# Optimization experiments

Hardware: AMD Instinct MI355X
Metric: run time of the kernel (lower is better)

The kernel has to match this reference:

```python
import jax, jax.numpy as jnp
import numpy as np

NUM_HEADS = 12
HEAD_DIM = 64
MAX_POS = 1024  # max_position_embeddings


def setup_inputs() -> dict:
    key = jax.random.key(0)
    ks = jax.random.split(key, 6)
    B, S, H = 4, 1024, 768
    return {
        "hidden_states": jax.random.normal(ks[0], (B, S, H), dtype=jnp.float32),
        "attention_mask": jnp.zeros((B, 1, 1, S), dtype=jnp.float32),
        "Wq": jax.random.normal(ks[1], (H, H), dtype=jnp.float32) * 0.02,
        "bq": jnp.zeros((H,), dtype=jnp.float32),
        "Wk": jax.random.normal(ks[2], (H, H), dtype=jnp.float32) * 0.02,
        "bk": jnp.zeros((H,), dtype=jnp.float32),
        "Wv": jax.random.normal(ks[3], (H, H), dtype=jnp.float32) * 0.02,
        "bv": jnp.zeros((H,), dtype=jnp.float32),
        "dist_emb": jax.random.normal(ks[4], (2 * MAX_POS - 1, HEAD_DIM), dtype=jnp.float32) * 0.02,
    }


def _split_heads(x):
    # [B, S, H] -> [B, nh, S, hd]
    B, S, _ = x.shape
    return x.reshape(B, S, NUM_HEADS, HEAD_DIM).transpose(0, 2, 1, 3)


def reference(hidden_states, attention_mask, Wq, bq, Wk, bk, Wv, bv, dist_emb):
    B, S, H = hidden_states.shape
    q = _split_heads(hidden_states @ Wq + bq)  # [B, nh, S, hd]
    k = _split_heads(hidden_states @ Wk + bk)
    v = _split_heads(hidden_states @ Wv + bv)

    # raw scores QK^T: [B, nh, S, S]
    scores = jnp.einsum("bhld,bhrd->bhlr", q, k)

    # relative_key_query positional bias
    dist = jnp.arange(S)[:, None] - jnp.arange(S)[None, :] + MAX_POS - 1  # [S, S]
    pos = dist_emb[dist]  # [S, S, hd]
    scores = scores + jnp.einsum("bhld,lrd->bhlr", q, pos) \
                    + jnp.einsum("bhrd,lrd->bhlr", k, pos)

    scores = scores / jnp.sqrt(jnp.asarray(HEAD_DIM, scores.dtype))
    scores = scores + attention_mask  # additive mask broadcast [B,1,1,S]

    probs = jax.nn.softmax(scores, axis=-1)  # dropout prob = 0.0 (eval)
    ctx = jnp.einsum("bhlr,bhrd->bhld", probs, v)  # [B, nh, S, hd]
    ctx = ctx.transpose(0, 2, 1, 3).reshape(B, S, H)
    return ctx
```

## Files before the change

kernel.cpp:

```cpp
#include <hip/hip_runtime.h>

#define SEQ 1024
#define NH  12
#define HD  64
#define HID 768
#define NB  4

#define LOG2E  1.4426950408889634f
#define SC2    0.18033688011112042f
#define DTHR   11.541560327111707f

typedef short bf16x8 __attribute__((ext_vector_type(8)));
typedef float f32x16 __attribute__((ext_vector_type(16)));

#define LBAR() do {                                             \
    __builtin_amdgcn_sched_barrier(0);                          \
    asm volatile("s_waitcnt lgkmcnt(0)" ::: "memory");          \
    __builtin_amdgcn_s_barrier();                               \
    __builtin_amdgcn_sched_barrier(0);                          \
} while (0)

__device__ __forceinline__ unsigned short f2b(float f) {
    union { float f; unsigned u; } v; v.f = f;
    unsigned r = (v.u + 0x7FFFu + ((v.u >> 16) & 1u)) >> 16;
    return (unsigned short)r;
}
__device__ __forceinline__ float b2f(unsigned short s) {
    union { unsigned u; float f; } v; v.u = (unsigned)s << 16;
    return v.f;
}
__device__ __forceinline__ float g4(const float4& v, int e) {
    return e == 0 ? v.x : e == 1 ? v.y : e == 2 ? v.z : v.w;
}
__device__ __forceinline__ unsigned short u16g(const ushort4& v, int e) {
    return e == 0 ? v.x : e == 1 ? v.y : e == 2 ? v.z : v.w;
}

#define ROWFN(r, h) (((r) & 3) + 8 * ((r) >> 2) + 4 * (h))

#define NX4 786432
#define NE4 32752

__global__ void cvt_all(const float* __restrict__ X, const float* __restrict__ E,
                        unsigned short* __restrict__ Xb, unsigned short* __restrict__ Eb) {
    int i = blockIdx.x * blockDim.x + threadIdx.x;
    const int stride = gridDim.x * blockDim.x;
    for (; i < NX4 + NE4; i += stride) {
        float4 v;
        if (i < NX4) v = ((const float4*)X)[i];
        else         v = ((const float4*)E)[i - NX4];
        ushort4 o;
        o.x = f2b(v.x); o.y = f2b(v.y); o.z = f2b(v.z); o.w = f2b(v.w);
        if (i < NX4) ((ushort4*)Xb)[i] = o;
        else         ((ushort4*)Eb)[i - NX4] = o;
    }
}

__global__ __launch_bounds__(256) void cvt_wt(
    const float* __restrict__ Wq, const float* __restrict__ Wk, const float* __restrict__ Wv,
    unsigned short* __restrict__ Wt)
{
    __shared__ float T[64][65];
    const int z = blockIdx.z;
    const float* __restrict__ W = (z == 0) ? Wq : (z == 1) ? Wk : Wv;
    const int k0 = blockIdx.x * 64, n0 = blockIdx.y * 64;
    const int tid = threadIdx.x;
    #pragma unroll
    for (int ir = 0; ir < 4; ++ir) {
        int r = ir * 16 + (tid >> 4);
        int c4 = (tid & 15) * 4;
        *(float4*)&T[r][c4] = *(const float4*)&W[(size_t)(k0 + r) * HID + n0 + c4];
    }
    __syncthreads();
    const int cc = tid >> 2, q = tid & 3;
    unsigned short* dst = Wt + (size_t)z * HID * HID + (size_t)(n0 + cc) * HID + k0 + q * 16;
    #pragma unroll
    for (int j4 = 0; j4 < 4; ++j4) {
        ushort4 t4;
        t4.x = f2b(T[q * 16 + j4 * 4 + 0][cc]);
        t4.y = f2b(T[q * 16 + j4 * 4 + 1][cc]);
        t4.z = f2b(T[q * 16 + j4 * 4 + 2][cc]);
        t4.w = f2b(T[q * 16 + j4 * 4 + 3][cc]);
        *(ushort4*)(dst + j4 * 4) = t4;
    }
}

__global__ __launch_bounds__(256) void gemm_qkv(
    const unsigned short* __restrict__ Xb,
    const unsigned short* __restrict__ Wt,
    const float* __restrict__ bq, const float* __restrict__ bk, const float* __restrict__ bv,
    unsigned short* __restrict__ qkv)
{
    __shared__ unsigned short Xs[128][64];
    __shared__ unsigned short Ws[128][64];

    const int tid = threadIdx.x;
    const int lane = tid & 63;
    const int wid = tid >> 6;
    const int c = lane & 31;
    const int h2 = lane >> 5;
    const int m0 = blockIdx.x * 128, N0 = blockIdx.y * 128, z = blockIdx.z;
    const unsigned short* __restrict__ Wz = Wt + (size_t)z * HID * HID;
    const float* __restrict__ bias = (z == 0) ? bq : (z == 1) ? bk : bv;

    f32x16 acc[2][2];
    #pragma unroll
    for (int i = 0; i < 2; ++i)
        #pragma unroll
        for (int j = 0; j < 2; ++j)
            #pragma unroll
            for (int r = 0; r < 16; ++r) acc[i][j][r] = 0.f;

    for (int k0 = 0; k0 < HID; k0 += 64) {
        __syncthreads();
        #pragma unroll
        for (int it = 0; it < 4; ++it) {
            int t16 = tid + 256 * it;
            int row = t16 >> 3, s = t16 & 7;
            bf16x8 xv = *(const bf16x8*)(Xb + (size_t)(m0 + row) * HID + k0 + s * 8);
            *(bf16x8*)&Xs[row][(s ^ (row & 7)) * 8] = xv;
            bf16x8 wv = *(const bf16x8*)(Wz + (size_t)(N0 + row) * HID + k0 + s * 8);
            *(bf16x8*)&Ws[row][(s ^ (row & 7)) * 8] = wv;
        }
        __syncthreads();
        #pragma unroll
        for (int kc = 0; kc < 4; ++kc) {
            const int slot = kc * 2 + h2;
            bf16x8 af[2], bf_[2];
            #pragma unroll
            for (int i = 0; i < 2; ++i) {
                int ar = 64 * (wid >> 1) + 32 * i + c;
                int br = 64 * (wid & 1) + 32 * i + c;
                if (z != 2) {
                    af[i]  = *(const bf16x8*)&Xs[ar][(slot ^ (ar & 7)) * 8];
                    bf_[i] = *(const bf16x8*)&Ws[br][(slot ^ (br & 7)) * 8];
                } else {
                    af[i]  = *(const bf16x8*)&Ws[ar][(slot ^ (ar & 7)) * 8];
                    bf_[i] = *(const bf16x8*)&Xs[br][(slot ^ (br & 7)) * 8];
                }
            }
            #pragma unroll
            for (int i = 0; i < 2; ++i)
                #pragma unroll
                for (int j = 0; j < 2; ++j)
                    acc[i][j] = __builtin_amdgcn_mfma_f32_32x32x16_bf16(af[i], bf_[j], acc[i][j], 0, 0, 0);
        }
    }

    unsigned short* outz = qkv + (size_t)z * (NB * SEQ * HID);
    if (z != 2) {
        #pragma unroll
        for (int j = 0; j < 2; ++j) {
            const int n = N0 + 64 * (wid & 1) + 32 * j + c;
            const float bv_ = bias[n];
            const int hh = n >> 6, d = n & 63;
            #pragma unroll
            for (int i = 0; i < 2; ++i) {
                #pragma unroll
                for (int r = 0; r < 16; ++r) {
                    int m = m0 + 64 * (wid >> 1) + 32 * i + ROWFN(r, h2);
                    int bb = m >> 10, ss = m & 1023;
                    outz[(((size_t)bb * NH + hh) * SEQ + ss) * HD + d] = f2b(acc[i][j][r] + bv_);
                }
            }
        }
    } else {
        #pragma unroll
        for (int i = 0; i < 2; ++i) {
            #pragma unroll
            for (int r = 0; r < 16; ++r) {
                int n = N0 + 64 * (wid >> 1) + 32 * i + ROWFN(r, h2);
                float bv_ = bias[n];
                int hh = n >> 6, d = n & 63;
                #pragma unroll
                for (int j = 0; j < 2; ++j) {
                    int m = m0 + 64 * (wid & 1) + 32 * j + c;
                    int bb = m >> 10, ss = m & 1023;
                    outz[(((size_t)bb * NH + hh) * HD + d) * SEQ + ss] = f2b(acc[i][j][r] + bv_);
                }
            }
        }
    }
}

__global__ __launch_bounds__(256, 2) void attn_mfma(
    const unsigned short* __restrict__ Qg,
    const unsigned short* __restrict__ Kg,
    const unsigned short* __restrict__ Vtg,
    const unsigned short* __restrict__ Eg,
    const float* __restrict__ mask,
    float* __restrict__ out)
{
    __shared__ float S1[64][68];
    __shared__ unsigned short MSS[64][76];
    __shared__ unsigned short NST[64][76];
    __shared__ unsigned short Pl[64][64];
    __shared__ float Corr[64];
    __shared__ float InvL[64];
    __shared__ int Fl[2];

    const int tid = threadIdx.x;
    const int lane = tid & 63;
    const int wid = tid >> 6;
    const int c = lane & 31;
    const int h2 = lane >> 5;
    const int RB = 32 * (wid >> 1);
    const int CB = 32 * (wid & 1);
    const int j0 = 64 * (wid & 1) + c;

    const int l0 = blockIdx.x * 64;
    const int bh = blockIdx.y;
    const int b = bh / NH;
    const int hh = bh - b * NH;

    const unsigned short* __restrict__ Qb = Qg + (size_t)bh * SEQ * HD;
    const unsigned short* __restrict__ Kb = Kg + (size_t)bh * SEQ * HD;
    const unsigned short* __restrict__ Vb = Vtg + (size_t)bh * HD * SEQ;
    const float* __restrict__ mrow_base = mask + (size_t)b * SEQ;

    if (tid < 2) Fl[tid] = 0;

    bf16x8 qa[4];
    #pragma unroll
    for (int kc = 0; kc < 4; ++kc)
        qa[kc] = *(const bf16x8*)(Qb + (size_t)(l0 + RB + c) * HD + kc * 16 + h2 * 8);

    f32x16 Oa;
    #pragma unroll
    for (int r = 0; r < 16; ++r) Oa[r] = 0.f;

    const int li = tid >> 2;
    const int c0q = (tid & 3) * 16;
    const int kli = (li ^ (li >> 3)) & 7;
    float m_run = -1e30f, lsum = 0.f;

    bf16x8 kb[4], ka[4], e0[4], e1[4], vb[4];
    {
        const int jr0 = l0 + 960 + j0;
        const int jra = jr0 > 2046 ? 2046 : jr0;
        const int jr1x = jr0 + 32;
        const int jrb = jr1x > 2046 ? 2046 : jr1x;
        #pragma unroll
        for (int kc = 0; kc < 4; ++kc) {
            kb[kc] = *(const bf16x8*)(Kb + (size_t)(CB + c) * HD + kc * 16 + h2 * 8);
            ka[kc] = *(const bf16x8*)(Kb + (size_t)(RB + c) * HD + kc * 16 + h2 * 8);
            e0[kc] = *(const bf16x8*)(Eg + (size_t)jra * HD + kc * 16 + h2 * 8);
            e1[kc] = *(const bf16x8*)(Eg + (size_t)jrb * HD + kc * 16 + h2 * 8);
            vb[kc] = *(const bf16x8*)(Vb + (size_t)(CB + c) * SEQ + kc * 16 + h2 * 8);
        }
    }

    for (int r0 = 0; r0 < SEQ; r0 += 64) {
        const int buf = (r0 >> 6) & 1;
        int r0n = r0 + 64; if (r0n >= SEQ) r0n = 0;

        float4 mk[4];
        #pragma unroll
        for (int q = 0; q < 4; ++q)
            mk[q] = *(const float4*)(mrow_base + r0 + c0q + 4 * q);

        {
            f32x16 s1a;
            #pragma unroll
            for (int r = 0; r < 16; ++r) s1a[r] = 0.f;
            __builtin_amdgcn_s_setprio(1);
            #pragma unroll
            for (int kc = 0; kc < 4; ++kc)
                s1a = __builtin_amdgcn_mfma_f32_32x32x16_bf16(qa[kc], kb[kc], s1a, 0, 0, 0);
            __builtin_amdgcn_s_setprio(0);
            #pragma unroll
            for (int rq = 0; rq < 16; ++rq)
                S1[RB + ROWFN(rq, h2)][CB + c] = s1a[rq];
        }
        #pragma unroll
        for (int kc = 0; kc < 4; ++kc)
            kb[kc] = *(const bf16x8*)(Kb + (size_t)(r0n + CB + c) * HD + kc * 16 + h2 * 8);
        __builtin_amdgcn_sched_barrier(0);

        {
            f32x16 ma0, na0;
            #pragma unroll
            for (int r = 0; r < 16; ++r) { ma0[r] = 0.f; na0[r] = 0.f; }
            __builtin_amdgcn_s_setprio(1);
            if (wid != 2) {
                #pragma unroll
                for (int kc = 0; kc < 4; ++kc)
                    ma0 = __builtin_amdgcn_mfma_f32_32x32x16_bf16(qa[kc], e0[kc], ma0, 0, 0, 0);
            }
            if (wid != 0) {
                #pragma unroll
                for (int kc = 0; kc < 4; ++kc)
                    na0 = __builtin_amdgcn_mfma_f32_32x32x16_bf16(ka[kc], e0[kc], na0, 0, 0, 0);
            }
            __builtin_amdgcn_s_setprio(0);
            if (wid != 2) {
                #pragma unroll
                for (int rq = 0; rq < 16; ++rq) {
                    const int lr = RB + ROWFN(rq, h2);
                    int rA = lr - j0 + 63;
                    if ((unsigned)rA < 64u) MSS[lr][rA] = f2b(ma0[rq]);
                }
            }
            if (wid != 0) {
                #pragma unroll
                for (int rq = 0; rq < 16; ++rq) {
                    const int lr = RB + ROWFN(rq, h2);
                    int lA = j0 + lr - 63;
                    if ((unsigned)lA < 64u) NST[lA][lr] = f2b(na0[rq]);
                }
            }
        }
        __builtin_amdgcn_sched_barrier(0);

        {
            f32x16 ma1, na1;
            #pragma unroll
            for (int r = 0; r < 16; ++r) { ma1[r] = 0.f; na1[r] = 0.f; }
            __builtin_amdgcn_s_setprio(1);
            if (wid != 1) {
                #pragma unroll
                for (int kc = 0; kc < 4; ++kc)
                    ma1 = __builtin_amdgcn_mfma_f32_32x32x16_bf16(qa[kc], e1[kc], ma1, 0, 0, 0);
            }
            if (wid != 3) {
                #pragma unroll
                for (int kc = 0; kc < 4; ++kc)
                    na1 = __builtin_amdgcn_mfma_f32_32x32x16_bf16(ka[kc], e1[kc], na1, 0, 0, 0);
            }
            __builtin_amdgcn_s_setprio(0);
            if (wid != 1) {
                #pragma unroll
                for (int rq = 0; rq < 16; ++rq) {
                    const int lr = RB + ROWFN(rq, h2);
                    int rB = lr - j0 + 31;
                    if ((unsigned)rB < 64u) MSS[lr][rB] = f2b(ma1[rq]);
                }
            }
            if (wid != 3) {
                #pragma unroll
                for (int rq = 0; rq < 16; ++rq) {
                    const int lr = RB + ROWFN(rq, h2);
                    int lB = j0 + lr - 31;
                    if ((unsigned)lB < 64u) NST[lB][lr] = f2b(na1[rq]);
                }
            }
        }
        __builtin_amdgcn_sched_barrier(0);

        {
            const int jr0n = l0 - r0n + 960 + j0;
            const int jran = jr0n > 2046 ? 2046 : jr0n;
            const int jr1n = jr0n + 32;
            const int jrbn = jr1n > 2046 ? 2046 : jr1n;
            #pragma unroll
            for (int kc = 0; kc < 4; ++kc) {
                ka[kc] = *(const bf16x8*)(Kb + (size_t)(r0n + RB + c) * HD + kc * 16 + h2 * 8);
                e0[kc] = *(const bf16x8*)(Eg + (size_t)jran * HD + kc * 16 + h2 * 8);
                e1[kc] = *(const bf16x8*)(Eg + (size_t)jrbn * HD + kc * 16 + h2 * 8);
            }
        }

        LBAR();

        float4 s4[4]; ushort4 mm[4], nn[4];
        #pragma unroll
        for (int q = 0; q < 4; ++q) {
            s4[q] = *(const float4*)&S1[li][c0q + 4 * q];
            mm[q] = *(const ushort4*)&MSS[li][c0q + 4 * q];
            nn[q] = *(const ushort4*)&NST[li][c0q + 4 * q];
        }
        float sc[16];
        #pragma unroll
        for (int j = 0; j < 16; ++j) {
            float mv = b2f(u16g(mm[j >> 2], j & 3));
            float nv = b2f(u16g(nn[j >> 2], j & 3));
            sc[j] = (g4(s4[j >> 2], j & 3) + mv + nv) * SC2 + g4(mk[j >> 2], j & 3) * LOG2E;
        }
        float tmax = sc[0];
        #pragma unroll
        for (int j = 1; j < 16; ++j) tmax = fmaxf(tmax, sc[j]);
        tmax = fmaxf(tmax, __shfl_xor(tmax, 1));
        tmax = fmaxf(tmax, __shfl_xor(tmax, 2));
        const bool upd = tmax > m_run + DTHR;
        const float m_new = upd ? tmax : m_run;
        const float corr = upd ? __builtin_amdgcn_exp2f(m_run - m_new) : 1.0f;
        if (upd) Fl[buf] = 1;
        float tsum = 0.f;
        unsigned short pb[16];
        #pragma unroll
        for (int j = 0; j < 16; ++j) {
            float p = __builtin_amdgcn_exp2f(sc[j] - m_new);
            tsum += p;
            pb[j] = f2b(p);
        }
        tsum += __shfl_xor(tsum, 1);
        tsum += __shfl_xor(tsum, 2);
        lsum = lsum * corr + tsum;
        m_run = m_new;
        if ((tid & 3) == 0) Corr[li] = corr;
        #pragma unroll
        for (int sblk = 0; sblk < 2; ++sblk) {
            bf16x8 pv;
            #pragma unroll
            for (int e = 0; e < 8; ++e) pv[e] = (short)pb[sblk * 8 + e];
            const int slot = ((c0q >> 3) + sblk) ^ kli;
            *(bf16x8*)&Pl[li][slot * 8] = pv;
        }

        LBAR();

        if (Fl[buf]) {
            #pragma unroll
            for (int q = 0; q < 4; ++q) {
                float4 cr = *(const float4*)&Corr[RB + 8 * q + 4 * h2];
                Oa[4 * q + 0] *= cr.x; Oa[4 * q + 1] *= cr.y;
                Oa[4 * q + 2] *= cr.z; Oa[4 * q + 3] *= cr.w;
            }
        }
        if (tid == 0) Fl[buf ^ 1] = 0;
        const int lrow = RB + c;
        const int klr = (lrow ^ (lrow >> 3)) & 7;
        __builtin_amdgcn_s_setprio(1);
        #pragma unroll
        for (int kc = 0; kc < 4; ++kc) {
            const int slot = kc * 2 + h2;
            bf16x8 pa = *(const bf16x8*)&Pl[lrow][(slot ^ klr) * 8];
            Oa = __builtin_amdgcn_mfma_f32_32x32x16_bf16(pa, vb[kc], Oa, 0, 0, 0);
        }
        __builtin_amdgcn_s_setprio(0);

        #pragma unroll
        for (int kc = 0; kc < 4; ++kc)
            vb[kc] = *(const bf16x8*)(Vb + (size_t)(CB + c) * SEQ + r0n + kc * 16 + h2 * 8);
    }

    if ((tid & 3) == 0) InvL[li] = 1.0f / lsum;
    __syncthreads();
    #pragma unroll
    for (int q = 0; q < 4; ++q) {
        float4 iv = *(const float4*)&InvL[RB + 8 * q + 4 * h2];
        #pragma unroll
        for (int e = 0; e < 4; ++e) {
            const int l = RB + 8 * q + 4 * h2 + e;
            out[((size_t)b * SEQ + l0 + l) * HID + hh * HD + CB + c] = Oa[4 * q + e] * g4(iv, e);
        }
    }
}

extern "C" void kernel_launch(void* const* d_in, const int* in_sizes, int n_in,
                              void* d_out, int out_size, void* d_ws, size_t ws_size,
                              hipStream_t stream) {
    const float* hidden = (const float*)d_in[0];
    const float* mask   = (const float*)d_in[1];
    const float* Wq     = (const float*)d_in[2];
    const float* bq     = (const float*)d_in[3];
    const float* Wk     = (const float*)d_in[4];
    const float* bk     = (const float*)d_in[5];
    const float* Wv     = (const float*)d_in[6];
    const float* bv     = (const float*)d_in[7];
    const float* E      = (const float*)d_in[8];
    float* outp = (float*)d_out;

    unsigned short* ws  = (unsigned short*)d_ws;
    unsigned short* Xbf = ws;
    unsigned short* Wt  = ws + 3145728;
    unsigned short* Ebf = ws + 4915200;
    unsigned short* qkv = ws + 5046272;

    cvt_all<<<dim3(1024), 256, 0, stream>>>(hidden, E, Xbf, Ebf);
    cvt_wt<<<dim3(12, 12, 3), 256, 0, stream>>>(Wq, Wk, Wv, Wt);
    gemm_qkv<<<dim3(32, 6, 3), 256, 0, stream>>>(Xbf, Wt, bq, bk, bv, qkv);
    const size_t per = (size_t)NB * SEQ * HID;
    attn_mfma<<<dim3(16, 48), 256, 0, stream>>>(qkv, qkv + per, qkv + 2 * per,
                                                Ebf, mask, outp);
}
```

Measured before the change: 178.0 us.

## Restructure PV stage so each wave owns its softmax rows, removing a barrier

The P·V product is rearranged so each wave computes output rows it produced softmax for, using 16x16x32 MFMAs. Rescale factors and the final normalisation now move through wave shuffles instead of shared Corr/InvL arrays and a flag. This removes the second block barrier per iteration. The QK score tile is stored as bf16, and S1/MSS/NST are double-buffered so the next iteration can write without a barrier. V tiles are staged through a double-buffered swizzled LDS buffer instead of per-wave registers. Costs are more LDS, extra precision loss on the raw scores, and a negative-index clamp on the embedding row prefetch.

Result: no change. 176.2 us (-1.0%).

```diff
diff --git a/kernel.cpp b/kernel.cpp
--- a/kernel.cpp
+++ b/kernel.cpp
@@ -12,6 +12,7 @@
 
 typedef short bf16x8 __attribute__((ext_vector_type(8)));
 typedef float f32x16 __attribute__((ext_vector_type(16)));
+typedef float f32x4  __attribute__((ext_vector_type(4)));
 
 #define LBAR() do {                                             \
     __builtin_amdgcn_sched_barrier(0);                          \
@@ -191,13 +192,11 @@
     const float* __restrict__ mask,
     float* __restrict__ out)
 {
-    __shared__ float S1[64][68];
-    __shared__ unsigned short MSS[64][76];
-    __shared__ unsigned short NST[64][76];
+    __shared__ unsigned short S1b[2][64][68];
+    __shared__ unsigned short MSS[2][64][68];
+    __shared__ unsigned short NST[2][64][68];
     __shared__ unsigned short Pl[64][64];
-    __shared__ float Corr[64];
-    __shared__ float InvL[64];
-    __shared__ int Fl[2];
+    __shared__ unsigned short Vt[2][64][64];
 
     const int tid = threadIdx.x;
     const int lane = tid & 63;
@@ -218,23 +217,28 @@
     const unsigned short* __restrict__ Vb = Vtg + (size_t)bh * HD * SEQ;
     const float* __restrict__ mrow_base = mask + (size_t)b * SEQ;
 
-    if (tid < 2) Fl[tid] = 0;
-
     bf16x8 qa[4];
     #pragma unroll
     for (int kc = 0; kc < 4; ++kc)
         qa[kc] = *(const bf16x8*)(Qb + (size_t)(l0 + RB + c) * HD + kc * 16 + h2 * 8);
 
-    f32x16 Oa;
-    #pragma unroll
-    for (int r = 0; r < 16; ++r) Oa[r] = 0.f;
+    f32x4 Oa4[4];
+    #pragma unroll
+    for (int dt = 0; dt < 4; ++dt)
+        #pragma unroll
+        for (int j = 0; j < 4; ++j) Oa4[dt][j] = 0.f;
 
     const int li = tid >> 2;
     const int c0q = (tid & 3) * 16;
     const int kli = (li ^ (li >> 3)) & 7;
+    const int vd0 = tid >> 3, vs8 = tid & 7;
+    const int kd0 = (vd0 ^ (vd0 >> 3)) & 7;
+    const int kd1 = ((vd0 + 32) ^ ((vd0 + 32) >> 3)) & 7;
+    const int pvrow = 16 * wid + (lane & 15);
+    const int kpl = (pvrow ^ (pvrow >> 3)) & 7;
     float m_run = -1e30f, lsum = 0.f;
 
-    bf16x8 kb[4], ka[4], e0[4], e1[4], vb[4];
+    bf16x8 kb[4], ka[4], e0[4], e1[4];
     {
         const int jr0 = l0 + 960 + j0;
         const int jra = jr0 > 2046 ? 2046 : jr0;
@@ -246,8 +250,11 @@
             ka[kc] = *(const bf16x8*)(Kb + (size_t)(RB + c) * HD + kc * 16 + h2 * 8);
             e0[kc] = *(const bf16x8*)(Eg + (size_t)jra * HD + kc * 16 + h2 * 8);
             e1[kc] = *(const bf16x8*)(Eg + (size_t)jrb * HD + kc * 16 + h2 * 8);
-            vb[kc] = *(const bf16x8*)(Vb + (size_t)(CB + c) * SEQ + kc * 16 + h2 * 8);
-        }
+        }
+        bf16x8 v0 = *(const bf16x8*)(Vb + (size_t)vd0 * SEQ + vs8 * 8);
+        bf16x8 v1 = *(const bf16x8*)(Vb + (size_t)(vd0 + 32) * SEQ + vs8 * 8);
+        *(bf16x8*)&Vt[0][vd0][(vs8 ^ kd0) * 8] = v0;
+        *(bf16x8*)&Vt[0][vd0 + 32][(vs8 ^ kd1) * 8] = v1;
     }
 
     for (int r0 = 0; r0 < SEQ; r0 += 64) {
@@ -258,6 +265,8 @@
         #pragma unroll
         for (int q = 0; q < 4; ++q)
             mk[q] = *(const float4*)(mrow_base + r0 + c0q + 4 * q);
+        bf16x8 vn0 = *(const bf16x8*)(Vb + (size_t)vd0 * SEQ + r0n + vs8 * 8);
+        bf16x8 vn1 = *(const bf16x8*)(Vb + (size_t)(vd0 + 32) * SEQ + r0n + vs8 * 8);
 
         {
             f32x16 s1a;
@@ -270,7 +279,7 @@
             __builtin_amdgcn_s_setprio(0);
             #pragma unroll
             for (int rq = 0; rq < 16; ++rq)
-                S1[RB + ROWFN(rq, h2)][CB + c] = s1a[rq];
+                S1b[buf][RB + ROWFN(rq, h2)][CB + c] = f2b(s1a[rq]);
         }
         #pragma unroll
         for (int kc = 0; kc < 4; ++kc)
@@ -298,7 +307,7 @@
                 for (int rq = 0; rq < 16; ++rq) {
                     const int lr = RB + ROWFN(rq, h2);
                     int rA = lr - j0 + 63;
-                    if ((unsigned)rA < 64u) MSS[lr][rA] = f2b(ma0[rq]);
+                    if ((unsigned)rA < 64u) MSS[buf][lr][rA] = f2b(ma0[rq]);
                 }
             }
             if (wid != 0) {
@@ -306,7 +315,7 @@
                 for (int rq = 0; rq < 16; ++rq) {
                     const int lr = RB + ROWFN(rq, h2);
                     int lA = j0 + lr - 63;
-                    if ((unsigned)lA < 64u) NST[lA][lr] = f2b(na0[rq]);
+                    if ((unsigned)lA < 64u) NST[buf][lA][lr] = f2b(na0[rq]);
                 }
             }
         }
@@ -333,7 +342,7 @@
                 for (int rq = 0; rq < 16; ++rq) {
                     const int lr = RB + ROWFN(rq, h2);
                     int rB = lr - j0 + 31;
-                    if ((unsigned)rB < 64u) MSS[lr][rB] = f2b(ma1[rq]);
+                    if ((unsigned)rB < 64u) MSS[buf][lr][rB] = f2b(ma1[rq]);
                 }
             }
             if (wid != 3) {
@@ -341,7 +350,7 @@
                 for (int rq = 0; rq < 16; ++rq) {
                     const int lr = RB + ROWFN(rq, h2);
                     int lB = j0 + lr - 31;
-                    if ((unsigned)lB < 64u) NST[lB][lr] = f2b(na1[rq]);
+                    if ((unsigned)lB < 64u) NST[buf][lB][lr] = f2b(na1[rq]);
                 }
             }
         }
@@ -349,9 +358,9 @@
 
         {
             const int jr0n = l0 - r0n + 960 + j0;
-            const int jran = jr0n > 2046 ? 2046 : jr0n;
+            const int jran = jr0n > 2046 ? 2046 : (jr0n < 0 ? 0 : jr0n);
             const int jr1n = jr0n + 32;
-            const int jrbn = jr1n > 2046 ? 2046 : jr1n;
+            const int jrbn = jr1n > 2046 ? 2046 : (jr1n < 0 ? 0 : jr1n);
             #pragma unroll
             for (int kc = 0; kc < 4; ++kc) {
                 ka[kc] = *(const bf16x8*)(Kb + (size_t)(r0n + RB + c) * HD + kc * 16 + h2 * 8);
@@ -362,19 +371,23 @@
 
         LBAR();
 
-        float4 s4[4]; ushort4 mm[4], nn[4];
+        *(bf16x8*)&Vt[buf ^ 1][vd0][(vs8 ^ kd0) * 8] = vn0;
+        *(bf16x8*)&Vt[buf ^ 1][vd0 + 32][(vs8 ^ kd1) * 8] = vn1;
+
+        ushort4 ss[4], mm[4], nn[4];
         #pragma unroll
         for (int q = 0; q < 4; ++q) {
-            s4[q] = *(const float4*)&S1[li][c0q + 4 * q];
-            mm[q] = *(const ushort4*)&MSS[li][c0q + 4 * q];
-            nn[q] = *(const ushort4*)&NST[li][c0q + 4 * q];
+            ss[q] = *(const ushort4*)&S1b[buf][li][c0q + 4 * q];
+            mm[q] = *(const ushort4*)&MSS[buf][li][c0q + 4 * q];
+            nn[q] = *(const ushort4*)&NST[buf][li][c0q + 4 * q];
         }
         float sc[16];
         #pragma unroll
         for (int j = 0; j < 16; ++j) {
+            float sv = b2f(u16g(ss[j >> 2], j & 3));
             float mv = b2f(u16g(mm[j >> 2], j & 3));
             float nv = b2f(u16g(nn[j >> 2], j & 3));
-            sc[j] = (g4(s4[j >> 2], j & 3) + mv + nv) * SC2 + g4(mk[j >> 2], j & 3) * LOG2E;
+            sc[j] = (sv + mv + nv) * SC2 + g4(mk[j >> 2], j & 3) * LOG2E;
         }
         float tmax = sc[0];
         #pragma unroll
@@ -384,7 +397,6 @@
         const bool upd = tmax > m_run + DTHR;
         const float m_new = upd ? tmax : m_run;
         const float corr = upd ? __builtin_amdgcn_exp2f(m_run - m_new) : 1.0f;
-        if (upd) Fl[buf] = 1;
         float tsum = 0.f;
         unsigned short pb[16];
         #pragma unroll
@@ -397,7 +409,6 @@
         tsum += __shfl_xor(tsum, 2);
         lsum = lsum * corr + tsum;
         m_run = m_new;
-        if ((tid & 3) == 0) Corr[li] = corr;
         #pragma unroll
         for (int sblk = 0; sblk < 2; ++sblk) {
             bf16x8 pv;
@@ -407,42 +418,54 @@
             *(bf16x8*)&Pl[li][slot * 8] = pv;
         }
 
-        LBAR();
-
-        if (Fl[buf]) {
-            #pragma unroll
-            for (int q = 0; q < 4; ++q) {
-                float4 cr = *(const float4*)&Corr[RB + 8 * q + 4 * h2];
-                Oa[4 * q + 0] *= cr.x; Oa[4 * q + 1] *= cr.y;
-                Oa[4 * q + 2] *= cr.z; Oa[4 * q + 3] *= cr.w;
-            }
-        }
-        if (tid == 0) Fl[buf ^ 1] = 0;
-        const int lrow = RB + c;
-        const int klr = (lrow ^ (lrow >> 3)) & 7;
+        asm volatile("s_waitcnt lgkmcnt(0)" ::: "memory");
+        __builtin_amdgcn_sched_barrier(0);
+
+        const unsigned long long wupd = __ballot(upd);
+        if (wupd) {
+            float cj[4];
+            #pragma unroll
+            for (int j = 0; j < 4; ++j)
+                cj[j] = __shfl(corr, (((lane >> 4) << 2) + j) << 2);
+            #pragma unroll
+            for (int dt = 0; dt < 4; ++dt) {
+                Oa4[dt][0] *= cj[0]; Oa4[dt][1] *= cj[1];
+                Oa4[dt][2] *= cj[2]; Oa4[dt][3] *= cj[3];
+            }
+        }
+        bf16x8 paf[2];
+        #pragma unroll
+        for (int rt = 0; rt < 2; ++rt) {
+            const int slot = ((rt << 2) + (lane >> 4)) ^ kpl;
+            paf[rt] = *(const bf16x8*)&Pl[pvrow][slot * 8];
+        }
         __builtin_amdgcn_s_setprio(1);
         #pragma unroll
-        for (int kc = 0; kc < 4; ++kc) {
-            const int slot = kc * 2 + h2;
-            bf16x8 pa = *(const bf16x8*)&Pl[lrow][(slot ^ klr) * 8];
-            Oa = __builtin_amdgcn_mfma_f32_32x32x16_bf16(pa, vb[kc], Oa, 0, 0, 0);
+        for (int dt = 0; dt < 4; ++dt) {
+            const int drow = dt * 16 + (lane & 15);
+            const int kdr = (drow ^ (drow >> 3)) & 7;
+            #pragma unroll
+            for (int rt = 0; rt < 2; ++rt) {
+                const int slot = ((rt << 2) + (lane >> 4)) ^ kdr;
+                bf16x8 vbf = *(const bf16x8*)&Vt[buf][drow][slot * 8];
+                Oa4[dt] = __builtin_amdgcn_mfma_f32_16x16x32_bf16(paf[rt], vbf, Oa4[dt], 0, 0, 0);
+            }
         }
         __builtin_amdgcn_s_setprio(0);
-
-        #pragma unroll
-        for (int kc = 0; kc < 4; ++kc)
-            vb[kc] = *(const bf16x8*)(Vb + (size_t)(CB + c) * SEQ + r0n + kc * 16 + h2 * 8);
-    }
-
-    if ((tid & 3) == 0) InvL[li] = 1.0f / lsum;
-    __syncthreads();
-    #pragma unroll
-    for (int q = 0; q < 4; ++q) {
-        float4 iv = *(const float4*)&InvL[RB + 8 * q + 4 * h2];
-        #pragma unroll
-        for (int e = 0; e < 4; ++e) {
-            const int l = RB + 8 * q + 4 * h2 + e;
-            out[((size_t)b * SEQ + l0 + l) * HID + hh * HD + CB + c] = Oa[4 * q + e] * g4(iv, e);
+    }
+
+    const float inv = 1.0f / lsum;
+    float ivj[4];
+    #pragma unroll
+    for (int j = 0; j < 4; ++j)
+        ivj[j] = __shfl(inv, (((lane >> 4) << 2) + j) << 2);
+    #pragma unroll
+    for (int dt = 0; dt < 4; ++dt) {
+        #pragma unroll
+        for (int j = 0; j < 4; ++j) {
+            const int l = 16 * wid + ((lane >> 4) << 2) + j;
+            out[((size_t)b * SEQ + l0 + l) * HID + hh * HD + dt * 16 + (lane & 15)] =
+                Oa4[dt][j] * ivj[j];
         }
     }
 }
```
